# Optimization experiments

Measured on AMD Instinct MI355X. Metric: run time of the kernel, lower is better.

## Reference

```python
import jax, jax.numpy as jnp
import numpy as np

N_NODES = 100000
N_EDGES = 3200000
IN_DIM = 128
HID = 64


def setup_inputs() -> dict:
    key = jax.random.key(0)
    ks = jax.random.split(key, 12)
    x = jax.random.normal(ks[0], (N_NODES, IN_DIM), dtype=jnp.float32)
    edge_index = jax.random.randint(ks[1], (2, N_EDGES), 0, N_NODES, dtype=jnp.int64)
    batch = jnp.zeros((N_NODES,), dtype=jnp.int64)
    s = 0.05
    params = {
        'fc_W': jax.random.normal(ks[2], (HID, IN_DIM), jnp.float32) * s,
        'fc_b': jnp.zeros((HID,), jnp.float32),
        # SAGEConv layer 1: lin_l (neighbor aggr, has bias), lin_r (root)
        'Wl1': jax.random.normal(ks[3], (HID, HID), jnp.float32) * s,
        'bl1': jnp.zeros((HID,), jnp.float32),
        'Wr1': jax.random.normal(ks[4], (HID, HID), jnp.float32) * s,
        # SAGEConv layer 2
        'Wl2': jax.random.normal(ks[5], (HID, HID), jnp.float32) * s,
        'bl2': jnp.zeros((HID,), jnp.float32),
        'Wr2': jax.random.normal(ks[6], (HID, HID), jnp.float32) * s,
        'head_W': jax.random.normal(ks[7], (1, HID), jnp.float32) * s,
        'head_b': jnp.zeros((1,), jnp.float32),
    }
    return {'x': x, 'edge_index': edge_index, 'batch': batch, **params}


def _sage_conv(h, src, dst, Wl, bl, Wr, n_nodes):
    # mean-aggregate neighbor features: gather over src, scatter-sum to dst
    msgs = h[src]                                            # [E, HID]
    agg = jax.ops.segment_sum(msgs, dst, num_segments=n_nodes)
    deg = jax.ops.segment_sum(jnp.ones((src.shape[0],), h.dtype), dst,
                              num_segments=n_nodes)
    agg = agg / jnp.maximum(deg, 1.0)[:, None]               # mean aggr
    return agg @ Wl.T + bl + h @ Wr.T                        # lin_l + lin_r


def reference(x, edge_index, batch, fc_W, fc_b, Wl1, bl1, Wr1, Wl2, bl2, Wr2,
              head_W, head_b):
    n_nodes = x.shape[0]
    src, dst = edge_index[0], edge_index[1]
    h = jax.nn.relu(x @ fc_W.T + fc_b)                       # fc + relu
    h = jax.nn.relu(_sage_conv(h, src, dst, Wl1, bl1, Wr1, n_nodes))  # SAGE 1 + relu
    h = _sage_conv(h, src, dst, Wl2, bl2, Wr2, n_nodes)      # SAGE 2 (no act)
    return h @ head_W.T + head_b                             # head -> [N, 1]
```

## Files before the change

### kernel.cpp

```cpp
#include <hip/hip_runtime.h>

#define N_NODES 100000
#define N_EDGES 3200000
#define IN_DIM 128
#define HID 64

#define NPB 32
#define NBUCK 3125
#define NBUCKP 3328
#define NBUCKP2 4096
#define TILE 12800
#define NSEG 250
#define RAWCAP 1408
#define FCB 391

typedef __attribute__((ext_vector_type(8))) short short8;
typedef __attribute__((ext_vector_type(4))) float f32x4;
typedef __attribute__((ext_vector_type(2))) float f32x2;

__device__ inline float bf2f(unsigned short u) {
    union { unsigned int u; float f; } c;
    c.u = ((unsigned int)u) << 16;
    return c.f;
}
__device__ inline unsigned short f2bf(float f) {
    union { float f; unsigned int u; } c;
    c.f = f;
    unsigned int u = c.u;
    return (unsigned short)((u + 0x7fffu + ((u >> 16) & 1u)) >> 16);
}
__device__ inline short8 cvt8(const float* __restrict__ p) {
    f32x4 lo = *reinterpret_cast<const f32x4*>(p);
    f32x4 hi = *reinterpret_cast<const f32x4*>(p + 4);
    short8 r;
#pragma unroll
    for (int j = 0; j < 4; ++j) { r[j] = (short)f2bf(lo[j]); r[4 + j] = (short)f2bf(hi[j]); }
    return r;
}
__device__ inline unsigned short pk_f8(float a, float b) {
    return (unsigned short)(__builtin_amdgcn_cvt_pk_fp8_f32(a, b, 0, false) & 0xffff);
}

__global__ __launch_bounds__(1024) void pre_kernel(
    const float* __restrict__ x, const float* __restrict__ fcW,
    const float* __restrict__ fcb, unsigned short* __restrict__ h0,
    unsigned char* __restrict__ h0f8,
    const int* __restrict__ ei, unsigned int* __restrict__ stage,
    int* __restrict__ offs,
    const float* __restrict__ Wl1, const float* __restrict__ Wr1,
    const float* __restrict__ Wl2, const float* __restrict__ Wr2,
    unsigned short* __restrict__ Wbf) {
    __shared__ int hoff[NBUCKP2];
    __shared__ int wsum[16];
    int tid = threadIdx.x;
    int lane = tid & 63, wid = tid >> 6;

    if (blockIdx.x < FCB) {
        int wtile = blockIdx.x * 16 + wid;
        if (wtile >= N_NODES / 16) return;
        int col = lane & 15, quad = lane >> 4;
        short8 bw[4][4];
#pragma unroll
        for (int nt = 0; nt < 4; ++nt)
#pragma unroll
            for (int ks = 0; ks < 4; ++ks)
                bw[nt][ks] = cvt8(fcW + (nt * 16 + col) * IN_DIM + ks * 32 + quad * 8);
        f32x4 acc[4];
#pragma unroll
        for (int nt = 0; nt < 4; ++nt) acc[nt] = {0.f, 0.f, 0.f, 0.f};
        int node0 = wtile * 16;
        const float* xrow = x + (size_t)(node0 + col) * IN_DIM + quad * 8;
#pragma unroll
        for (int ks = 0; ks < 4; ++ks) {
            short8 a = cvt8(xrow + ks * 32);
#pragma unroll
            for (int nt = 0; nt < 4; ++nt)
                acc[nt] = __builtin_amdgcn_mfma_f32_16x16x32_bf16(a, bw[nt][ks], acc[nt], 0, 0, 0);
        }
#pragma unroll
        for (int nt = 0; nt < 4; ++nt) {
            float bias = fcb[nt * 16 + col];
#pragma unroll
            for (int r = 0; r < 4; ++r) {
                float v = acc[nt][r] + bias;
                v = v > 0.f ? v : 0.f;
                int node = node0 + quad * 4 + r;
                int f = nt * 16 + col;
                h0[(size_t)node * HID + f] = f2bf(v);
                float w = __shfl_xor(v, 1);
                if (!(col & 1))
                    *(unsigned short*)(h0f8 + (size_t)node * HID + f) = pk_f8(v, w);
            }
        }
    } else if (blockIdx.x < FCB + NSEG) {
        int blk = blockIdx.x - FCB;
        int e0 = blk * TILE;
        for (int i = tid; i < NBUCKP2; i += 1024) hoff[i] = 0;
        __syncthreads();
        for (int i = tid; i < TILE; i += 1024)
            atomicAdd(&hoff[ei[(size_t)N_EDGES + e0 + i] >> 5], 1);
        __syncthreads();
        int base = tid * 4;
        int vals[4];
        int s = 0;
#pragma unroll
        for (int j = 0; j < 4; ++j) { vals[j] = s; s += hoff[base + j]; }
        int inc = s;
#pragma unroll
        for (int d = 1; d < 64; d <<= 1) {
            int n = __shfl_up(inc, d);
            if (lane >= d) inc += n;
        }
        int wave_excl = inc - s;
        if (lane == 63) wsum[wid] = inc;
        __syncthreads();
        if (tid == 0) {
            int r = 0;
#pragma unroll
            for (int w = 0; w < 16; ++w) { int t = wsum[w]; wsum[w] = r; r += t; }
        }
        __syncthreads();
        int tbase = wsum[wid] + wave_excl;
        __syncthreads();
#pragma unroll
        for (int j = 0; j < 4; ++j) hoff[base + j] = tbase + vals[j];
        __syncthreads();
        int* og = offs + (size_t)blk * NBUCKP;
        for (int i = tid; i < NBUCKP; i += 1024) og[i] = hoff[i];
        __syncthreads();
        unsigned int* sg = stage + (size_t)blk * TILE;
        for (int i = tid; i < TILE; i += 1024) {
            int idx = e0 + i;
            int src = ei[idx];
            int dst = ei[(size_t)N_EDGES + idx];
            int pos = atomicAdd(&hoff[dst >> 5], 1);
            sg[pos] = ((unsigned int)src << 5) | (unsigned int)(dst & 31);
        }
    } else {
        const float* mats[4] = {Wl1, Wr1, Wl2, Wr2};
#pragma unroll
        for (int m = 0; m < 4; ++m)
            for (int i = tid; i < HID * HID; i += 1024)
                Wbf[m * HID * HID + i] = f2bf(mats[m][i]);
    }
}

__global__ __launch_bounds__(256) void agg_sage(
    const unsigned short* __restrict__ h, const unsigned char* __restrict__ h8,
    const unsigned int* __restrict__ stage, const int* __restrict__ offs,
    const unsigned short* __restrict__ Wlb, const unsigned short* __restrict__ Wrb,
    const float* __restrict__ bl, const float* __restrict__ hw,
    const float* __restrict__ hbias,
    unsigned short* __restrict__ h_out, unsigned char* __restrict__ h8_out,
    float* __restrict__ head_out, int do_head) {
    __shared__ unsigned int raw[RAWCAP];
    __shared__ unsigned int srt[RAWCAP];
    __shared__ unsigned int aggT[NPB][36];
    __shared__ int bcnt[256], bpos[256], bstart[256];
    __shared__ int cnt32[NPB], off32[NPB];
    __shared__ int wsum[4];
    __shared__ int seg_alloc;
    __shared__ float headacc[NPB];
    int tid = threadIdx.x;
    int lane = tid & 63, wid = tid >> 6;
    int b = blockIdx.x;

    if (tid == 0) seg_alloc = 0;
    if (tid < NPB) headacc[tid] = 0.f;
    bcnt[tid] = 0;
    __syncthreads();

    if (tid < NSEG) {
        const int* ob = offs + (size_t)tid * NBUCKP + b;
        int s2 = ob[0], e2 = ob[1];
        int n = e2 - s2;
        if (n > 0) {
            int p = atomicAdd(&seg_alloc, n);
            if (p + n > RAWCAP) n = (RAWCAP > p) ? (RAWCAP - p) : 0;
            const unsigned int* sp = stage + (size_t)tid * TILE + s2;
            for (int i = 0; i < n; ++i) raw[p + i] = sp[i];
        }
    }
    __syncthreads();
    int total = seg_alloc;
    if (total > RAWCAP) total = RAWCAP;

    for (int i = tid; i < total; i += 256)
        atomicAdd(&bcnt[((raw[i] & 31) << 3) | (raw[i] >> 19)], 1);
    __syncthreads();
    {
        int v = bcnt[tid];
        int s = v;
#pragma unroll
        for (int d = 1; d < 64; d <<= 1) {
            int n = __shfl_up(s, d);
            if (lane >= d) s += n;
        }
        if (lane == 63) wsum[wid] = s;
        __syncthreads();
        if (tid == 0) {
            int r = 0;
#pragma unroll
            for (int w = 0; w < 4; ++w) { int t = wsum[w]; wsum[w] = r; r += t; }
        }
        __syncthreads();
        int excl = wsum[wid] + s - v;
        bstart[tid] = excl;
        bpos[tid] = excl;
    }
    __syncthreads();
    if (tid < NPB) {
        int o = bstart[tid * 8];
        int e = (tid == NPB - 1) ? total : bstart[(tid + 1) * 8];
        off32[tid] = o;
        cnt32[tid] = e - o;
    }
    __syncthreads();
    for (int i = tid; i < total; i += 256) {
        unsigned int u = raw[i];
        int p = atomicAdd(&bpos[((u & 31) << 3) | (u >> 19)], 1);
        srt[p] = u >> 5;
    }
    __syncthreads();

    int q = lane >> 4, f4 = lane & 15;
#pragma unroll
    for (int k = 0; k < 8; ++k) {
        int d = wid * 8 + k;
        int s = off32[d], n = cnt32[d];
        float a0 = 0.f, a1 = 0.f, a2 = 0.f, a3 = 0.f;
        int i = 0;
        for (; i + 16 <= n; i += 16) {
            unsigned int e0 = srt[s + i + q];
            unsigned int e1 = srt[s + i + 4 + q];
            unsigned int e2 = srt[s + i + 8 + q];
            unsigned int e3 = srt[s + i + 12 + q];
            unsigned int g0 = *(const unsigned int*)(h8 + (size_t)e0 * HID + f4 * 4);
            unsigned int g1 = *(const unsigned int*)(h8 + (size_t)e1 * HID + f4 * 4);
            unsigned int g2 = *(const unsigned int*)(h8 + (size_t)e2 * HID + f4 * 4);
            unsigned int g3 = *(const unsigned int*)(h8 + (size_t)e3 * HID + f4 * 4);
            f32x2 lo, hi;
            lo = __builtin_amdgcn_cvt_pk_f32_fp8(g0, false);
            hi = __builtin_amdgcn_cvt_pk_f32_fp8(g0, true);
            a0 += lo.x; a1 += lo.y; a2 += hi.x; a3 += hi.y;
            lo = __builtin_amdgcn_cvt_pk_f32_fp8(g1, false);
            hi = __builtin_amdgcn_cvt_pk_f32_fp8(g1, true);
            a0 += lo.x; a1 += lo.y; a2 += hi.x; a3 += hi.y;
            lo = __builtin_amdgcn_cvt_pk_f32_fp8(g2, false);
            hi = __builtin_amdgcn_cvt_pk_f32_fp8(g2, true);
            a0 += lo.x; a1 += lo.y; a2 += hi.x; a3 += hi.y;
            lo = __builtin_amdgcn_cvt_pk_f32_fp8(g3, false);
            hi = __builtin_amdgcn_cvt_pk_f32_fp8(g3, true);
            a0 += lo.x; a1 += lo.y; a2 += hi.x; a3 += hi.y;
        }
        for (; i < n; i += 4) {
            int valid = (i + q) < n;
            unsigned int e = srt[valid ? (s + i + q) : s];
            unsigned int g = *(const unsigned int*)(h8 + (size_t)e * HID + f4 * 4);
            if (valid) {
                f32x2 lo = __builtin_amdgcn_cvt_pk_f32_fp8(g, false);
                f32x2 hi = __builtin_amdgcn_cvt_pk_f32_fp8(g, true);
                a0 += lo.x; a1 += lo.y; a2 += hi.x; a3 += hi.y;
            }
        }
        a0 += __shfl_xor(a0, 16); a0 += __shfl_xor(a0, 32);
        a1 += __shfl_xor(a1, 16); a1 += __shfl_xor(a1, 32);
        a2 += __shfl_xor(a2, 16); a2 += __shfl_xor(a2, 32);
        a3 += __shfl_xor(a3, 16); a3 += __shfl_xor(a3, 32);
        if (q == 0) {
            float inv = n > 0 ? 1.f / (float)n : 0.f;
            aggT[d][f4 * 2] = (unsigned int)f2bf(a0 * inv) |
                              ((unsigned int)f2bf(a1 * inv) << 16);
            aggT[d][f4 * 2 + 1] = (unsigned int)f2bf(a2 * inv) |
                                  ((unsigned int)f2bf(a3 * inv) << 16);
        }
    }
    __syncthreads();

    {
        int t = wid >> 1, np = wid & 1;
        int col = lane & 15, quad = lane >> 4;
        int m = t * 16 + col;
        int node0 = b * NPB;

        short8 aggA[2], hinA[2];
        const unsigned short* aggrow = (const unsigned short*)&aggT[m][0];
#pragma unroll
        for (int ks = 0; ks < 2; ++ks) {
            aggA[ks] = *reinterpret_cast<const short8*>(aggrow + ks * 32 + quad * 8);
            hinA[ks] = *reinterpret_cast<const short8*>(
                h + (size_t)(node0 + m) * HID + ks * 32 + quad * 8);
        }
        short8 bwl[2][2], bwr[2][2];
#pragma unroll
        for (int nt = 0; nt < 2; ++nt) {
            int f = np * 32 + nt * 16 + col;
#pragma unroll
            for (int ks = 0; ks < 2; ++ks) {
                bwl[nt][ks] = *reinterpret_cast<const short8*>(
                    Wlb + (size_t)f * HID + ks * 32 + quad * 8);
                bwr[nt][ks] = *reinterpret_cast<const short8*>(
                    Wrb + (size_t)f * HID + ks * 32 + quad * 8);
            }
        }
        f32x4 acc[2];
#pragma unroll
        for (int nt = 0; nt < 2; ++nt) acc[nt] = {0.f, 0.f, 0.f, 0.f};
#pragma unroll
        for (int ks = 0; ks < 2; ++ks) {
#pragma unroll
            for (int nt = 0; nt < 2; ++nt) {
                acc[nt] = __builtin_amdgcn_mfma_f32_16x16x32_bf16(aggA[ks], bwl[nt][ks], acc[nt], 0, 0, 0);
                acc[nt] = __builtin_amdgcn_mfma_f32_16x16x32_bf16(hinA[ks], bwr[nt][ks], acc[nt], 0, 0, 0);
            }
        }

        if (!do_head) {
#pragma unroll
            for (int nt = 0; nt < 2; ++nt) {
                int f = np * 32 + nt * 16 + col;
                float bias = bl[f];
#pragma unroll
                for (int r = 0; r < 4; ++r) {
                    float v = acc[nt][r] + bias;
                    v = v > 0.f ? v : 0.f;
                    int node = node0 + t * 16 + quad * 4 + r;
                    h_out[(size_t)node * HID + f] = f2bf(v);
                    float w = __shfl_xor(v, 1);
                    if (!(col & 1))
                        *(unsigned short*)(h8_out + (size_t)node * HID + f) = pk_f8(v, w);
                }
            }
        } else {
            float vr[4] = {0.f, 0.f, 0.f, 0.f};
#pragma unroll
            for (int nt = 0; nt < 2; ++nt) {
                int f = np * 32 + nt * 16 + col;
                float w = hw[f], bias = bl[f];
#pragma unroll
                for (int r = 0; r < 4; ++r) vr[r] += (acc[nt][r] + bias) * w;
            }
#pragma unroll
            for (int r = 0; r < 4; ++r) {
#pragma unroll
                for (int d = 1; d < 16; d <<= 1) vr[r] += __shfl_xor(vr[r], d);
            }
            if (col == 0) {
#pragma unroll
                for (int r = 0; r < 4; ++r)
                    atomicAdd(&headacc[t * 16 + quad * 4 + r], vr[r]);
            }
            __syncthreads();
            if (tid < NPB) head_out[node0 + tid] = headacc[tid] + hbias[0];
        }
    }
}

extern "C" void kernel_launch(void* const* d_in, const int* in_sizes, int n_in,
                              void* d_out, int out_size, void* d_ws, size_t ws_size,
                              hipStream_t stream) {
    const float* x   = (const float*)d_in[0];
    const int*   ei  = (const int*)d_in[1];
    const float* fcW = (const float*)d_in[3];
    const float* fcb = (const float*)d_in[4];
    const float* Wl1 = (const float*)d_in[5];
    const float* bl1 = (const float*)d_in[6];
    const float* Wr1 = (const float*)d_in[7];
    const float* Wl2 = (const float*)d_in[8];
    const float* bl2 = (const float*)d_in[9];
    const float* Wr2 = (const float*)d_in[10];
    const float* hW  = (const float*)d_in[11];
    const float* hb  = (const float*)d_in[12];
    float* out = (float*)d_out;

    char* ws = (char*)d_ws;
    size_t off = 0;
    auto alloc = [&](size_t bytes) -> char* {
        char* p = ws + off;
        off = (off + bytes + 255) & ~(size_t)255;
        return p;
    };
    unsigned short* h0   = (unsigned short*)alloc((size_t)N_NODES * HID * 2);
    unsigned short* h1   = (unsigned short*)alloc((size_t)N_NODES * HID * 2);
    unsigned char*  h0f8 = (unsigned char*)alloc((size_t)N_NODES * HID);
    unsigned char*  h1f8 = (unsigned char*)alloc((size_t)N_NODES * HID);
    unsigned int* stage  = (unsigned int*)alloc((size_t)N_EDGES * 4);
    int* offs            = (int*)alloc((size_t)NSEG * NBUCKP * 4);
    unsigned short* Wbf  = (unsigned short*)alloc((size_t)4 * HID * HID * 2);

    pre_kernel<<<FCB + NSEG + 1, 1024, 0, stream>>>(
        x, fcW, fcb, h0, h0f8, ei, stage, offs, Wl1, Wr1, Wl2, Wr2, Wbf);
    agg_sage<<<NBUCK, 256, 0, stream>>>(h0, h0f8, stage, offs,
                                        Wbf, Wbf + HID * HID, bl1,
                                        nullptr, nullptr, h1, h1f8, nullptr, 0);
    agg_sage<<<NBUCK, 256, 0, stream>>>(h1, h1f8, stage, offs,
                                        Wbf + 2 * HID * HID, Wbf + 3 * HID * HID, bl2,
                                        hW, hb, nullptr, nullptr, out, 1);
}
```

Baseline: 345.1 us.

## Cache per-bucket sorted edge lists from layer 1 for reuse in layer 2

```diff
diff --git a/kernel.cpp b/kernel.cpp
--- a/kernel.cpp
+++ b/kernel.cpp
@@ -95,10 +95,18 @@
     } else if (blockIdx.x < FCB + NSEG) {
         int blk = blockIdx.x - FCB;
         int e0 = blk * TILE;
+        int sd[13], ss[13];
         for (int i = tid; i < NBUCKP2; i += 1024) hoff[i] = 0;
         __syncthreads();
-        for (int i = tid; i < TILE; i += 1024)
-            atomicAdd(&hoff[ei[(size_t)N_EDGES + e0 + i] >> 5], 1);
+#pragma unroll
+        for (int k = 0; k < 13; ++k) {
+            int i = tid + k * 1024;
+            if (i < TILE) {
+                sd[k] = ei[(size_t)N_EDGES + e0 + i];
+                ss[k] = ei[e0 + i];
+                atomicAdd(&hoff[sd[k] >> 5], 1);
+            }
+        }
         __syncthreads();
         int base = tid * 4;
         int vals[4];
@@ -129,12 +137,13 @@
         for (int i = tid; i < NBUCKP; i += 1024) og[i] = hoff[i];
         __syncthreads();
         unsigned int* sg = stage + (size_t)blk * TILE;
-        for (int i = tid; i < TILE; i += 1024) {
-            int idx = e0 + i;
-            int src = ei[idx];
-            int dst = ei[(size_t)N_EDGES + idx];
-            int pos = atomicAdd(&hoff[dst >> 5], 1);
-            sg[pos] = ((unsigned int)src << 5) | (unsigned int)(dst & 31);
+#pragma unroll
+        for (int k = 0; k < 13; ++k) {
+            int i = tid + k * 1024;
+            if (i < TILE) {
+                int pos = atomicAdd(&hoff[sd[k] >> 5], 1);
+                sg[pos] = ((unsigned int)ss[k] << 5) | (unsigned int)(sd[k] & 31);
+            }
         }
     } else {
         const float* mats[4] = {Wl1, Wr1, Wl2, Wr2};
@@ -148,80 +157,69 @@
 __global__ __launch_bounds__(256) void agg_sage(
     const unsigned short* __restrict__ h, const unsigned char* __restrict__ h8,
     const unsigned int* __restrict__ stage, const int* __restrict__ offs,
+    unsigned int* __restrict__ g_srt, int* __restrict__ g_cnt,
     const unsigned short* __restrict__ Wlb, const unsigned short* __restrict__ Wrb,
     const float* __restrict__ bl, const float* __restrict__ hw,
     const float* __restrict__ hbias,
     unsigned short* __restrict__ h_out, unsigned char* __restrict__ h8_out,
-    float* __restrict__ head_out, int do_head) {
+    float* __restrict__ head_out, int do_head, int mode) {
     __shared__ unsigned int raw[RAWCAP];
     __shared__ unsigned int srt[RAWCAP];
     __shared__ unsigned int aggT[NPB][36];
-    __shared__ int bcnt[256], bpos[256], bstart[256];
-    __shared__ int cnt32[NPB], off32[NPB];
-    __shared__ int wsum[4];
+    __shared__ int cnt32[NPB], off32[NPB], pos32[NPB];
     __shared__ int seg_alloc;
     __shared__ float headacc[NPB];
     int tid = threadIdx.x;
     int lane = tid & 63, wid = tid >> 6;
     int b = blockIdx.x;
 
-    if (tid == 0) seg_alloc = 0;
-    if (tid < NPB) headacc[tid] = 0.f;
-    bcnt[tid] = 0;
-    __syncthreads();
-
-    if (tid < NSEG) {
-        const int* ob = offs + (size_t)tid * NBUCKP + b;
-        int s2 = ob[0], e2 = ob[1];
-        int n = e2 - s2;
-        if (n > 0) {
-            int p = atomicAdd(&seg_alloc, n);
-            if (p + n > RAWCAP) n = (RAWCAP > p) ? (RAWCAP - p) : 0;
-            const unsigned int* sp = stage + (size_t)tid * TILE + s2;
-            for (int i = 0; i < n; ++i) raw[p + i] = sp[i];
-        }
-    }
-    __syncthreads();
-    int total = seg_alloc;
-    if (total > RAWCAP) total = RAWCAP;
-
-    for (int i = tid; i < total; i += 256)
-        atomicAdd(&bcnt[((raw[i] & 31) << 3) | (raw[i] >> 19)], 1);
-    __syncthreads();
-    {
-        int v = bcnt[tid];
-        int s = v;
-#pragma unroll
-        for (int d = 1; d < 64; d <<= 1) {
-            int n = __shfl_up(s, d);
-            if (lane >= d) s += n;
-        }
-        if (lane == 63) wsum[wid] = s;
+    if (mode == 0) {
+        if (tid == 0) seg_alloc = 0;
+        if (tid < NPB) { cnt32[tid] = 0; headacc[tid] = 0.f; }
+        __syncthreads();
+        if (tid < NSEG) {
+            const int* ob = offs + (size_t)tid * NBUCKP + b;
+            int s2 = ob[0], e2 = ob[1];
+            int n = e2 - s2;
+            if (n > 0) {
+                int p = atomicAdd(&seg_alloc, n);
+                if (p + n > RAWCAP) n = (RAWCAP > p) ? (RAWCAP - p) : 0;
+                const unsigned int* sp = stage + (size_t)tid * TILE + s2;
+                for (int i = 0; i < n; ++i) raw[p + i] = sp[i];
+            }
+        }
+        __syncthreads();
+        int total = seg_alloc;
+        if (total > RAWCAP) total = RAWCAP;
+        for (int i = tid; i < total; i += 256) atomicAdd(&cnt32[raw[i] & 31], 1);
         __syncthreads();
         if (tid == 0) {
             int r = 0;
-#pragma unroll
-            for (int w = 0; w < 4; ++w) { int t = wsum[w]; wsum[w] = r; r += t; }
-        }
-        __syncthreads();
-        int excl = wsum[wid] + s - v;
-        bstart[tid] = excl;
-        bpos[tid] = excl;
+            for (int j = 0; j < NPB; ++j) { off32[j] = r; pos32[j] = r; r += cnt32[j]; }
+        }
+        __syncthreads();
+        for (int i = tid; i < total; i += 256) {
+            unsigned int u = raw[i];
+            int p = atomicAdd(&pos32[u & 31], 1);
+            srt[p] = u >> 5;
+        }
+        __syncthreads();
+        for (int i = tid; i < total; i += 256) g_srt[(size_t)b * RAWCAP + i] = srt[i];
+        if (tid < NPB) {
+            g_cnt[b * 64 + tid] = cnt32[tid];
+            g_cnt[b * 64 + 32 + tid] = off32[tid];
+        }
+    } else {
+        if (tid < NPB) {
+            cnt32[tid] = g_cnt[b * 64 + tid];
+            off32[tid] = g_cnt[b * 64 + 32 + tid];
+            headacc[tid] = 0.f;
+        }
+        __syncthreads();
+        int total = off32[NPB - 1] + cnt32[NPB - 1];
+        for (int i = tid; i < total; i += 256) srt[i] = g_srt[(size_t)b * RAWCAP + i];
+        __syncthreads();
     }
-    __syncthreads();
-    if (tid < NPB) {
-        int o = bstart[tid * 8];
-        int e = (tid == NPB - 1) ? total : bstart[(tid + 1) * 8];
-        off32[tid] = o;
-        cnt32[tid] = e - o;
-    }
-    __syncthreads();
-    for (int i = tid; i < total; i += 256) {
-        unsigned int u = raw[i];
-        int p = atomicAdd(&bpos[((u & 31) << 3) | (u >> 19)], 1);
-        srt[p] = u >> 5;
-    }
-    __syncthreads();
 
     int q = lane >> 4, f4 = lane & 15;
 #pragma unroll
@@ -230,28 +228,33 @@
         int s = off32[d], n = cnt32[d];
         float a0 = 0.f, a1 = 0.f, a2 = 0.f, a3 = 0.f;
         int i = 0;
+        for (; i + 32 <= n; i += 32) {
+            unsigned int g[8];
+#pragma unroll
+            for (int j = 0; j < 8; ++j) {
+                unsigned int e = srt[s + i + j * 4 + q];
+                g[j] = *(const unsigned int*)(h8 + (size_t)e * HID + f4 * 4);
+            }
+#pragma unroll
+            for (int j = 0; j < 8; ++j) {
+                f32x2 lo = __builtin_amdgcn_cvt_pk_f32_fp8(g[j], false);
+                f32x2 hi = __builtin_amdgcn_cvt_pk_f32_fp8(g[j], true);
+                a0 += lo.x; a1 += lo.y; a2 += hi.x; a3 += hi.y;
+            }
+        }
         for (; i + 16 <= n; i += 16) {
-            unsigned int e0 = srt[s + i + q];
-            unsigned int e1 = srt[s + i + 4 + q];
-            unsigned int e2 = srt[s + i + 8 + q];
-            unsigned int e3 = srt[s + i + 12 + q];
-            unsigned int g0 = *(const unsigned int*)(h8 + (size_t)e0 * HID + f4 * 4);
-            unsigned int g1 = *(const unsigned int*)(h8 + (size_t)e1 * HID + f4 * 4);
-            unsigned int g2 = *(const unsigned int*)(h8 + (size_t)e2 * HID + f4 * 4);
-            unsigned int g3 = *(const unsigned int*)(h8 + (size_t)e3 * HID + f4 * 4);
-            f32x2 lo, hi;
-            lo = __builtin_amdgcn_cvt_pk_f32_fp8(g0, false);
-            hi = __builtin_amdgcn_cvt_pk_f32_fp8(g0, true);
-            a0 += lo.x; a1 += lo.y; a2 += hi.x; a3 += hi.y;
-            lo = __builtin_amdgcn_cvt_pk_f32_fp8(g1, false);
-            hi = __builtin_amdgcn_cvt_pk_f32_fp8(g1, true);
-            a0 += lo.x; a1 += lo.y; a2 += hi.x; a3 += hi.y;
-            lo = __builtin_amdgcn_cvt_pk_f32_fp8(g2, false);
-            hi = __builtin_amdgcn_cvt_pk_f32_fp8(g2, true);
-            a0 += lo.x; a1 += lo.y; a2 += hi.x; a3 += hi.y;
-            lo = __builtin_amdgcn_cvt_pk_f32_fp8(g3, false);
-            hi = __builtin_amdgcn_cvt_pk_f32_fp8(g3, true);
-            a0 += lo.x; a1 += lo.y; a2 += hi.x; a3 += hi.y;
+            unsigned int g[4];
+#pragma unroll
+            for (int j = 0; j < 4; ++j) {
+                unsigned int e = srt[s + i + j * 4 + q];
+                g[j] = *(const unsigned int*)(h8 + (size_t)e * HID + f4 * 4);
+            }
+#pragma unroll
+            for (int j = 0; j < 4; ++j) {
+                f32x2 lo = __builtin_amdgcn_cvt_pk_f32_fp8(g[j], false);
+                f32x2 hi = __builtin_amdgcn_cvt_pk_f32_fp8(g[j], true);
+                a0 += lo.x; a1 += lo.y; a2 += hi.x; a3 += hi.y;
+            }
         }
         for (; i < n; i += 4) {
             int valid = (i + q) < n;
@@ -386,14 +389,16 @@
     unsigned char*  h1f8 = (unsigned char*)alloc((size_t)N_NODES * HID);
     unsigned int* stage  = (unsigned int*)alloc((size_t)N_EDGES * 4);
     int* offs            = (int*)alloc((size_t)NSEG * NBUCKP * 4);
+    unsigned int* g_srt  = (unsigned int*)alloc((size_t)NBUCK * RAWCAP * 4);
+    int* g_cnt           = (int*)alloc((size_t)NBUCK * 64 * 4);
     unsigned short* Wbf  = (unsigned short*)alloc((size_t)4 * HID * HID * 2);
 
     pre_kernel<<<FCB + NSEG + 1, 1024, 0, stream>>>(
         x, fcW, fcb, h0, h0f8, ei, stage, offs, Wl1, Wr1, Wl2, Wr2, Wbf);
-    agg_sage<<<NBUCK, 256, 0, stream>>>(h0, h0f8, stage, offs,
+    agg_sage<<<NBUCK, 256, 0, stream>>>(h0, h0f8, stage, offs, g_srt, g_cnt,
                                         Wbf, Wbf + HID * HID, bl1,
-                                        nullptr, nullptr, h1, h1f8, nullptr, 0);
-    agg_sage<<<NBUCK, 256, 0, stream>>>(h1, h1f8, stage, offs,
+                                        nullptr, nullptr, h1, h1f8, nullptr, 0, 0);
+    agg_sage<<<NBUCK, 256, 0, stream>>>(h1, h1f8, stage, offs, g_srt, g_cnt,
                                         Wbf + 2 * HID * HID, Wbf + 3 * HID * HID, bl2,
-                                        hW, hb, nullptr, nullptr, out, 1);
-}
+                                        hW, hb, nullptr, nullptr, out, 1, 1);
+}
```

Measured after the change: 292.8 us. 15.2% less time.
